# Kernel optimization log

Measured on AMD Instinct MI355X. Metric: run time of the kernel, lower is better.

Reference implementation:

```python
import jax, jax.numpy as jnp
import numpy as np

N_NODES = 100000
N_EDGES = 600000
IN_DIM = 128
HID = 128
OUT_DIM = 64
N_LAYERS = 3


def setup_inputs() -> dict:
    key = jax.random.key(0)
    ks = jax.random.split(key, 8)
    x = jax.random.normal(ks[0], (N_NODES, IN_DIM), dtype=jnp.float32)
    edge_index = jax.random.randint(ks[1], (2, N_EDGES), 0, N_NODES, dtype=jnp.int64)
    s = 1.0 / np.sqrt(HID)
    W_in = jax.random.normal(ks[2], (HID, IN_DIM), dtype=jnp.float32) * s
    b_in = jax.random.normal(ks[3], (HID,), dtype=jnp.float32) * s
    W_convs = jax.random.normal(ks[4], (N_LAYERS, HID, HID), dtype=jnp.float32) * s
    b_convs = jax.random.normal(ks[5], (N_LAYERS, HID), dtype=jnp.float32) * s
    W_out = jax.random.normal(ks[6], (OUT_DIM, (N_LAYERS + 1) * HID), dtype=jnp.float32) * s
    b_out = jax.random.normal(ks[7], (OUT_DIM,), dtype=jnp.float32) * s
    return {"x": x, "edge_index": edge_index, "W_in": W_in, "b_in": b_in,
            "W_convs": W_convs, "b_convs": b_convs, "W_out": W_out, "b_out": b_out}


def reference(x, edge_index, W_in, b_in, W_convs, b_convs, W_out, b_out):
    src, dst = edge_index[0], edge_index[1]
    n = x.shape[0]
    # input projection: [N, in] -> [N, H]
    h = x @ W_in.T + b_in
    hidden_states = [h]
    for i in range(W_convs.shape[0]):
        # GINConv (eps=0): nn(x + sum of neighbor messages), messages src->dst
        agg = jax.ops.segment_sum(h[src], dst, num_segments=n)
        h = (h + agg) @ W_convs[i].T + b_convs[i]
        hidden_states.append(h)
    cat = jnp.concatenate(hidden_states, axis=1)  # [N, (L+1)*H]
    out = cat @ W_out.T + b_out  # [N, OUT]
    return jax.nn.softmax(out, axis=-1)
```

## Files before the change

kernel.cpp:

```cpp
#include <hip/hip_runtime.h>
#include <hip/hip_bf16.h>
#include <hip/hip_fp16.h>

#define GN 100000
#define GE 600000
#define SCAN_NBLK 98
#define ALD 132
#define EDGE_BLOCKS ((GE + 255) / 256)
#define CONV_BLOCKS ((81984 + 255) / 256)

typedef __bf16    bf16x8 __attribute__((ext_vector_type(8)));
typedef _Float16  f16x8  __attribute__((ext_vector_type(8)));
typedef float     f32x4  __attribute__((ext_vector_type(4)));

__global__ __launch_bounds__(256) void prep_fused(
    const int* __restrict__ dst, int* __restrict__ deg,
    const float* __restrict__ Win, const float* __restrict__ Wc,
    const float* __restrict__ Wout,
    const float* __restrict__ b3, const float* __restrict__ bOut,
    __bf16* __restrict__ hi, __bf16* __restrict__ lo,
    float* __restrict__ cvec)
{
    if (blockIdx.x < EDGE_BLOCKS) {
        const int e = blockIdx.x * 256 + threadIdx.x;
        if (e < GE) atomicAdd(&deg[dst[e]], 1);
        return;
    }
    const int i = (blockIdx.x - EDGE_BLOCKS) * 256 + threadIdx.x;
    const float* W3 = Wc + 32768;
    if (i >= 81984) return;
    if (i >= 81920) {
        const int o = i - 81920;
        float c = bOut[o];
        for (int j = 0; j < 128; ++j)
            c += Wout[o * 512 + 384 + j] * b3[j];
        cvec[o] = c;
        return;
    }
    float v;
    if (i < 16384) {
        v = Win[i];
    } else if (i < 49152) {
        v = Wc[i - 16384];
    } else if (i < 57344) {
        const int j = i - 49152;
        v = Wout[(j >> 7) * 512 + (j & 127)];
    } else if (i < 65536) {
        const int j = i - 57344;
        v = Wout[(j >> 7) * 512 + 128 + (j & 127)];
    } else if (i < 73728) {
        const int j = i - 65536;
        v = Wout[(j >> 7) * 512 + 256 + (j & 127)];
    } else {
        const int j = i - 65536;
        const int o = (j >> 7) - 64;
        const int k = j & 127;
        float s = 0.f;
        for (int jj = 0; jj < 128; ++jj)
            s += Wout[o * 512 + 384 + jj] * W3[jj * 128 + k];
        v = s;
    }
    const __bf16 h = (__bf16)v;
    hi[i] = h;
    lo[i] = (__bf16)(v - (float)h);
}

__global__ __launch_bounds__(256) void scan_pass1(const int* __restrict__ deg,
                                                  int* __restrict__ excl,
                                                  int* __restrict__ blockSums,
                                                  int* __restrict__ blockOffs,
                                                  int* __restrict__ done)
{
    __shared__ int s[256];
    __shared__ bool amLast;
    const int t = threadIdx.x;
    const int base = blockIdx.x * 1024 + t * 4;

    int4 v = make_int4(0, 0, 0, 0);
    if (base + 3 < GN) {
        v = *(const int4*)(deg + base);
    } else {
        if (base + 0 < GN) v.x = deg[base + 0];
        if (base + 1 < GN) v.y = deg[base + 1];
        if (base + 2 < GN) v.z = deg[base + 2];
        if (base + 3 < GN) v.w = deg[base + 3];
    }
    const int mysum = v.x + v.y + v.z + v.w;
    s[t] = mysum;
    __syncthreads();
    for (int off = 1; off < 256; off <<= 1) {
        const int val = (t >= off) ? s[t - off] : 0;
        __syncthreads();
        s[t] += val;
        __syncthreads();
    }
    int4 o;
    o.x = s[t] - mysum;
    o.y = o.x + v.x;
    o.z = o.y + v.y;
    o.w = o.z + v.z;
    if (base + 3 < GN) {
        *(int4*)(excl + base) = o;
    } else {
        if (base + 0 < GN) excl[base + 0] = o.x;
        if (base + 1 < GN) excl[base + 1] = o.y;
        if (base + 2 < GN) excl[base + 2] = o.z;
        if (base + 3 < GN) excl[base + 3] = o.w;
    }
    if (t == 255) blockSums[blockIdx.x] = s[255];

    __threadfence();
    if (t == 0)
        amLast = (atomicAdd(done, 1) == SCAN_NBLK - 1);
    __syncthreads();
    if (amLast) {
        __threadfence();
        const int bv = (t < SCAN_NBLK) ? blockSums[t] : 0;
        s[t] = (t < 128) ? bv : 0;
        __syncthreads();
        for (int off = 1; off < 128; off <<= 1) {
            const int val = (t >= off && t < 128) ? s[t - off] : 0;
            __syncthreads();
            if (t < 128) s[t] += val;
            __syncthreads();
        }
        if (t < SCAN_NBLK) blockOffs[t] = s[t] - bv;
    }
}

__global__ __launch_bounds__(256, 8) void gather_rows(
    const uint* __restrict__ Hw,
    const int* __restrict__ row_start,
    const int* __restrict__ deg,
    const int* __restrict__ csr,
    float* __restrict__ Aggp)
{
    const int wave = threadIdx.x >> 6;
    const int lane = threadIdx.x & 63;
    const int row  = blockIdx.x * 4 + wave;
    if (row >= GN) return;

    const uint self = Hw[(size_t)row * 64 + lane];
    const int start = row_start[row];
    const int dg    = deg[row];
    float2 acc = make_float2(0.f, 0.f);

    for (int b = 0; b < dg; b += 64) {
        const int n = min(dg - b, 64);
        const int idx = csr[start + min(b + lane, dg - 1)];
        for (int k = 0; k < n; k += 8) {
            uint t[8];
#pragma unroll
            for (int u = 0; u < 8; ++u) {
                const int s = __shfl(idx, min(k + u, n - 1));
                t[u] = Hw[(size_t)s * 64 + lane];
            }
            const int m = min(n - k, 8);
#pragma unroll
            for (int u = 0; u < 8; ++u) {
                if (u < m) {
                    union { uint uu; _Float16 h[2]; } cv;
                    cv.uu = t[u];
                    acc.x += (float)cv.h[0];
                    acc.y += (float)cv.h[1];
                }
            }
        }
    }

    union { uint uu; _Float16 h[2]; } sv;
    sv.uu = self;
    acc.x += (float)sv.h[0];
    acc.y += (float)sv.h[1];

    *(float2*)&Aggp[(size_t)row * 128 + lane * 2] = acc;
}

__global__ __launch_bounds__(256, 8) void gather_softmax(
    const float* __restrict__ Y,
    const int* __restrict__ row_start,
    const int* __restrict__ deg,
    const int* __restrict__ csr,
    const float* __restrict__ P0,
    const float* __restrict__ P1,
    const float* __restrict__ P2,
    const float* __restrict__ cvec,
    float* __restrict__ out)
{
    const int wave = threadIdx.x >> 6;
    const int lane = threadIdx.x & 63;
    const int row  = blockIdx.x * 4 + wave;
    if (row >= GN) return;

    const size_t g = (size_t)row * 64 + lane;
    const float p0 = P0[g];
    const float p1 = P1[g];
    const float p2 = P2[g];
    const float self = Y[g];
    const float cv = cvec[lane];

    const int start = row_start[row];
    const int dg    = deg[row];
    float acc = 0.f;

    for (int b = 0; b < dg; b += 64) {
        const int n = min(dg - b, 64);
        const int idx = csr[start + min(b + lane, dg - 1)];
        for (int k = 0; k < n; k += 8) {
            float t[8];
#pragma unroll
            for (int u = 0; u < 8; ++u) {
                const int s = __shfl(idx, min(k + u, n - 1));
                t[u] = Y[(size_t)s * 64 + lane];
            }
            const int m = min(n - k, 8);
#pragma unroll
            for (int u = 0; u < 8; ++u)
                if (u < m) acc += t[u];
        }
    }

    const float v = p0 + p1 + p2 + (acc + self) + cv;
    float mx = v;
#pragma unroll
    for (int off = 32; off > 0; off >>= 1) mx = fmaxf(mx, __shfl_xor(mx, off));
    const float e = __expf(v - mx);
    float s = e;
#pragma unroll
    for (int off = 32; off > 0; off >>= 1) s += __shfl_xor(s, off);
    out[g] = e / s;
}

__device__ __forceinline__ void gemm_tile(
    const float* __restrict__ AccBuf,
    const __bf16* __restrict__ Whi, const __bf16* __restrict__ Wlo,
    const int wn, const int quad, const int l15,
    f32x4 acc[2][2])
{
#pragma unroll
    for (int i = 0; i < 2; ++i)
#pragma unroll
        for (int j = 0; j < 2; ++j) acc[i][j] = (f32x4)(0.0f);

    bf16x8 whA[2], wlA[2], whB[2], wlB[2];
#pragma unroll
    for (int nt = 0; nt < 2; ++nt) {
        const int n = wn + nt * 16 + l15;
        whA[nt] = *(const bf16x8*)(Whi + (size_t)n * 128 + quad * 8);
        wlA[nt] = *(const bf16x8*)(Wlo + (size_t)n * 128 + quad * 8);
    }
#pragma unroll
    for (int ks = 0; ks < 4; ++ks) {
        const int kt = ks * 32 + quad * 8;
        if (ks < 3) {
            const int kn = kt + 32;
#pragma unroll
            for (int nt = 0; nt < 2; ++nt) {
                const int n = wn + nt * 16 + l15;
                whB[nt] = *(const bf16x8*)(Whi + (size_t)n * 128 + kn);
                wlB[nt] = *(const bf16x8*)(Wlo + (size_t)n * 128 + kn);
            }
        }
        bf16x8 ahi[2], alo[2];
#pragma unroll
        for (int mt = 0; mt < 2; ++mt) {
            const float* ap = &AccBuf[(mt * 16 + l15) * ALD + kt];
            const f32x4 p = *(const f32x4*)ap;
            const f32x4 q = *(const f32x4*)(ap + 4);
#pragma unroll
            for (int e = 0; e < 4; ++e) {
                const __bf16 hp = (__bf16)p[e];
                const __bf16 hq = (__bf16)q[e];
                ahi[mt][e]     = hp;
                ahi[mt][e + 4] = hq;
                alo[mt][e]     = (__bf16)(p[e] - (float)hp);
                alo[mt][e + 4] = (__bf16)(q[e] - (float)hq);
            }
        }
#pragma unroll
        for (int mt = 0; mt < 2; ++mt)
#pragma unroll
            for (int nt = 0; nt < 2; ++nt) {
                acc[mt][nt] = __builtin_amdgcn_mfma_f32_16x16x32_bf16(
                    ahi[mt], whA[nt], acc[mt][nt], 0, 0, 0);
                acc[mt][nt] = __builtin_amdgcn_mfma_f32_16x16x32_bf16(
                    ahi[mt], wlA[nt], acc[mt][nt], 0, 0, 0);
                acc[mt][nt] = __builtin_amdgcn_mfma_f32_16x16x32_bf16(
                    alo[mt], whA[nt], acc[mt][nt], 0, 0, 0);
            }
        if (ks < 3) {
#pragma unroll
            for (int nt = 0; nt < 2; ++nt) {
                whA[nt] = whB[nt];
                wlA[nt] = wlB[nt];
            }
        }
    }
}

__device__ __forceinline__ void gemm_tile64(
    const float* __restrict__ AccBuf,
    const __bf16* __restrict__ Ehi, const __bf16* __restrict__ Elo,
    const int wn16, const int quad, const int l15,
    f32x4 acc[2])
{
    acc[0] = (f32x4)(0.0f);
    acc[1] = (f32x4)(0.0f);

    const int n = wn16 + l15;
    bf16x8 whA, wlA, whB, wlB;
    whA = *(const bf16x8*)(Ehi + (size_t)n * 128 + quad * 8);
    wlA = *(const bf16x8*)(Elo + (size_t)n * 128 + quad * 8);

#pragma unroll
    for (int ks = 0; ks < 4; ++ks) {
        const int kt = ks * 32 + quad * 8;
        if (ks < 3) {
            whB = *(const bf16x8*)(Ehi + (size_t)n * 128 + kt + 32);
            wlB = *(const bf16x8*)(Elo + (size_t)n * 128 + kt + 32);
        }
        bf16x8 ahi[2], alo[2];
#pragma unroll
        for (int mt = 0; mt < 2; ++mt) {
            const float* ap = &AccBuf[(mt * 16 + l15) * ALD + kt];
            const f32x4 p = *(const f32x4*)ap;
            const f32x4 q = *(const f32x4*)(ap + 4);
#pragma unroll
            for (int e = 0; e < 4; ++e) {
                const __bf16 hp = (__bf16)p[e];
                const __bf16 hq = (__bf16)q[e];
                ahi[mt][e]     = hp;
                ahi[mt][e + 4] = hq;
                alo[mt][e]     = (__bf16)(p[e] - (float)hp);
                alo[mt][e + 4] = (__bf16)(q[e] - (float)hq);
            }
        }
#pragma unroll
        for (int mt = 0; mt < 2; ++mt) {
            acc[mt] = __builtin_amdgcn_mfma_f32_16x16x32_bf16(
                ahi[mt], whA, acc[mt], 0, 0, 0);
            acc[mt] = __builtin_amdgcn_mfma_f32_16x16x32_bf16(
                ahi[mt], wlA, acc[mt], 0, 0, 0);
            acc[mt] = __builtin_amdgcn_mfma_f32_16x16x32_bf16(
                alo[mt], whA, acc[mt], 0, 0, 0);
        }
        if (ks < 3) { whA = whB; wlA = wlB; }
    }
}

template<int MODE>
__global__ __launch_bounds__(256, 3) void gin_layer(
    const float* __restrict__ in,
    const __bf16* __restrict__ Whi,
    const __bf16* __restrict__ Wlo,
    const float* __restrict__ bias,
    const __bf16* __restrict__ Ehi,
    const __bf16* __restrict__ Elo,
    _Float16* __restrict__ Hout,
    float* __restrict__ partial,
    float* __restrict__ y2)
{
    __shared__ float Acc[32 * ALD];

    const int tid  = threadIdx.x;
    const int wave = tid >> 6;
    const int lane = tid & 63;
    const int row0 = blockIdx.x * 32;
    const int wn   = wave * 32;
    const int quad = lane >> 4;
    const int l15  = lane & 15;
    const int c8   = l15 * 8;

#pragma unroll
    for (int p = 0; p < 2; ++p) {
        const int r = wave * 8 + p * 4 + quad;
        const size_t g = (size_t)(row0 + r) * 128 + c8;
        const f32x4 v0 = *(const f32x4*)(in + g);
        const f32x4 v1 = *(const f32x4*)(in + g + 4);
        *(f32x4*)&Acc[r * ALD + c8]     = v0;
        *(f32x4*)&Acc[r * ALD + c8 + 4] = v1;
    }
    __syncthreads();

    f32x4 acc1[2][2];
    gemm_tile(Acc, Whi, Wlo, wn, quad, l15, acc1);
    __syncthreads();

#pragma unroll
    for (int nt = 0; nt < 2; ++nt) {
        const int col = wn + nt * 16 + l15;
        const float b = bias[col];
#pragma unroll
        for (int mt = 0; mt < 2; ++mt)
#pragma unroll
            for (int r4 = 0; r4 < 4; ++r4)
                Acc[(mt * 16 + quad * 4 + r4) * ALD + col] = acc1[mt][nt][r4] + b;
    }
    __syncthreads();

    if (MODE < 2) {
#pragma unroll
        for (int p = 0; p < 2; ++p) {
            const int q = tid + p * 256;
            const int r = q >> 4;
            const int g = (q & 15) * 8;
            const float4 a = *(const float4*)&Acc[r * ALD + g];
            const float4 b = *(const float4*)&Acc[r * ALD + g + 4];
            f16x8 o = {(_Float16)a.x, (_Float16)a.y, (_Float16)a.z, (_Float16)a.w,
                       (_Float16)b.x, (_Float16)b.y, (_Float16)b.z, (_Float16)b.w};
            *(f16x8*)&Hout[(size_t)(row0 + r) * 128 + g] = o;
        }
    }

    if (MODE < 2) {
        f32x4 accE[2];
        gemm_tile64(Acc, Ehi, Elo, wave * 16, quad, l15, accE);
        const int colE = wave * 16 + l15;
#pragma unroll
        for (int mt = 0; mt < 2; ++mt)
#pragma unroll
            for (int r4 = 0; r4 < 4; ++r4)
                partial[(size_t)(row0 + mt * 16 + quad * 4 + r4) * 64 + colE]
                    = accE[mt][r4];
    } else {
        f32x4 acc2[2][2];
        gemm_tile(Acc, Ehi, Elo, wn, quad, l15, acc2);
        float* const dst = (wave < 2) ? partial : y2;
        const int cbase = wn & 63;
#pragma unroll
        for (int nt = 0; nt < 2; ++nt)
#pragma unroll
            for (int mt = 0; mt < 2; ++mt)
#pragma unroll
                for (int r4 = 0; r4 < 4; ++r4)
                    dst[(size_t)(row0 + mt * 16 + quad * 4 + r4) * 64
                        + cbase + nt * 16 + l15] = acc2[mt][nt][r4];
    }
}

__global__ __launch_bounds__(256) void scan_pass3(int* __restrict__ excl,
                                                  const int* __restrict__ blockOffs,
                                                  int* __restrict__ cursor)
{
    const int i = blockIdx.x * 256 + threadIdx.x;
    if (i >= GN) return;
    const int v = excl[i] + blockOffs[i >> 10];
    excl[i]   = v;
    cursor[i] = v;
}

__global__ __launch_bounds__(256) void fill_csr(const int* __restrict__ src,
                                                const int* __restrict__ dst,
                                                int* __restrict__ cursor,
                                                int* __restrict__ csr)
{
    const int e = blockIdx.x * 256 + threadIdx.x;
    if (e >= GE) return;
    const int pos = atomicAdd(&cursor[dst[e]], 1);
    csr[pos] = src[e];
}

extern "C" void kernel_launch(void* const* d_in, const int* in_sizes, int n_in,
                              void* d_out, int out_size, void* d_ws, size_t ws_size,
                              hipStream_t stream)
{
    const float* x       = (const float*)d_in[0];
    const int*   src     = (const int*)d_in[1];
    const int*   dst     = ((const int*)d_in[1]) + GE;
    const float* W_in    = (const float*)d_in[2];
    const float* b_in    = (const float*)d_in[3];
    const float* W_convs = (const float*)d_in[4];
    const float* b_convs = (const float*)d_in[5];
    const float* W_out   = (const float*)d_in[6];
    const float* b_out   = (const float*)d_in[7];
    float*       out     = (float*)d_out;

    _Float16* h0   = (_Float16*)d_ws;
    _Float16* h1   = h0 + (size_t)GN * 128;
    float*    Aggp = (float*)(h1 + (size_t)GN * 128);
    float*    p0   = Aggp + (size_t)GN * 128;
    float*    p1   = p0 + (size_t)GN * 64;
    float*    p2   = p1 + (size_t)GN * 64;
    float*    y2   = p2 + (size_t)GN * 64;
    float*    cvec = y2 + (size_t)GN * 64;
    int*      deg       = (int*)(cvec + 128);
    int*      done      = deg + GN;
    int*      row_start = done + 4;
    int*      cursor    = row_start + GN;
    int*      blockSums = cursor + GN;
    int*      blockOffs = blockSums + 128;
    int*      csr       = blockOffs + 128;
    __bf16*   Whi       = (__bf16*)(csr + GE);
    __bf16*   Wlo       = Whi + 81920;

    const dim3 blk(256);
    const dim3 gblk(256);
    const int node_blocks   = (GN + 255) / 256;
    const int layer_blocks  = GN / 32;
    const int gather_blocks = (GN + 3) / 4;

    hipMemsetAsync(deg, 0, (GN + 4) * sizeof(int), stream);
    prep_fused<<<EDGE_BLOCKS + CONV_BLOCKS, blk, 0, stream>>>(
        dst, deg, W_in, W_convs, W_out, b_convs + 256, b_out, Whi, Wlo, cvec);
    scan_pass1<<<SCAN_NBLK, blk, 0, stream>>>(deg, row_start, blockSums,
                                              blockOffs, done);
    scan_pass3<<<node_blocks, blk, 0, stream>>>(row_start, blockOffs, cursor);
    fill_csr<<<EDGE_BLOCKS, blk, 0, stream>>>(src, dst, cursor, csr);

    gin_layer<0><<<layer_blocks, gblk, 0, stream>>>(
        x, Whi, Wlo, b_in, Whi + 49152, Wlo + 49152, h0, p0, nullptr);

    gather_rows<<<gather_blocks, gblk, 0, stream>>>(
        (const uint*)h0, row_start, deg, csr, Aggp);
    gin_layer<1><<<layer_blocks, gblk, 0, stream>>>(
        Aggp, Whi + 16384, Wlo + 16384, b_convs,
        Whi + 57344, Wlo + 57344, h1, p1, nullptr);

    gather_rows<<<gather_blocks, gblk, 0, stream>>>(
        (const uint*)h1, row_start, deg, csr, Aggp);
    gin_layer<2><<<layer_blocks, gblk, 0, stream>>>(
        Aggp, Whi + 32768, Wlo + 32768, b_convs + 128,
        Whi + 65536, Wlo + 65536, nullptr, p2, y2);

    gather_softmax<<<gather_blocks, gblk, 0, stream>>>(
        y2, row_start, deg, csr, p0, p1, p2, cvec, out);
}
```

Baseline: 442.7 us.

## Fuse input projection layer into prep kernel using on-the-fly fp32 weight splitting

```diff
diff --git a/kernel.cpp b/kernel.cpp
--- a/kernel.cpp
+++ b/kernel.cpp
@@ -8,61 +8,298 @@
 #define ALD 132
 #define EDGE_BLOCKS ((GE + 255) / 256)
 #define CONV_BLOCKS ((81984 + 255) / 256)
+#define L0_BLOCKS   (GN / 32)
 
 typedef __bf16    bf16x8 __attribute__((ext_vector_type(8)));
 typedef _Float16  f16x8  __attribute__((ext_vector_type(8)));
 typedef float     f32x4  __attribute__((ext_vector_type(4)));
 
-__global__ __launch_bounds__(256) void prep_fused(
+__device__ __forceinline__ void split8(const float* __restrict__ wp,
+                                       bf16x8& hi, bf16x8& lo)
+{
+    const f32x4 a = *(const f32x4*)wp;
+    const f32x4 b = *(const f32x4*)(wp + 4);
+#pragma unroll
+    for (int e = 0; e < 4; ++e) {
+        const __bf16 ha = (__bf16)a[e];
+        const __bf16 hb = (__bf16)b[e];
+        hi[e]     = ha;
+        hi[e + 4] = hb;
+        lo[e]     = (__bf16)(a[e] - (float)ha);
+        lo[e + 4] = (__bf16)(b[e] - (float)hb);
+    }
+}
+
+__device__ __forceinline__ void gemm_tile(
+    const float* __restrict__ AccBuf,
+    const __bf16* __restrict__ Whi, const __bf16* __restrict__ Wlo,
+    const int wn, const int quad, const int l15,
+    f32x4 acc[2][2])
+{
+#pragma unroll
+    for (int i = 0; i < 2; ++i)
+#pragma unroll
+        for (int j = 0; j < 2; ++j) acc[i][j] = (f32x4)(0.0f);
+
+    bf16x8 whA[2], wlA[2], whB[2], wlB[2];
+#pragma unroll
+    for (int nt = 0; nt < 2; ++nt) {
+        const int n = wn + nt * 16 + l15;
+        whA[nt] = *(const bf16x8*)(Whi + (size_t)n * 128 + quad * 8);
+        wlA[nt] = *(const bf16x8*)(Wlo + (size_t)n * 128 + quad * 8);
+    }
+#pragma unroll
+    for (int ks = 0; ks < 4; ++ks) {
+        const int kt = ks * 32 + quad * 8;
+        if (ks < 3) {
+            const int kn = kt + 32;
+#pragma unroll
+            for (int nt = 0; nt < 2; ++nt) {
+                const int n = wn + nt * 16 + l15;
+                whB[nt] = *(const bf16x8*)(Whi + (size_t)n * 128 + kn);
+                wlB[nt] = *(const bf16x8*)(Wlo + (size_t)n * 128 + kn);
+            }
+        }
+        bf16x8 ahi[2], alo[2];
+#pragma unroll
+        for (int mt = 0; mt < 2; ++mt) {
+            const float* ap = &AccBuf[(mt * 16 + l15) * ALD + kt];
+            const f32x4 p = *(const f32x4*)ap;
+            const f32x4 q = *(const f32x4*)(ap + 4);
+#pragma unroll
+            for (int e = 0; e < 4; ++e) {
+                const __bf16 hp = (__bf16)p[e];
+                const __bf16 hq = (__bf16)q[e];
+                ahi[mt][e]     = hp;
+                ahi[mt][e + 4] = hq;
+                alo[mt][e]     = (__bf16)(p[e] - (float)hp);
+                alo[mt][e + 4] = (__bf16)(q[e] - (float)hq);
+            }
+        }
+#pragma unroll
+        for (int mt = 0; mt < 2; ++mt)
+#pragma unroll
+            for (int nt = 0; nt < 2; ++nt) {
+                acc[mt][nt] = __builtin_amdgcn_mfma_f32_16x16x32_bf16(
+                    ahi[mt], whA[nt], acc[mt][nt], 0, 0, 0);
+                acc[mt][nt] = __builtin_amdgcn_mfma_f32_16x16x32_bf16(
+                    ahi[mt], wlA[nt], acc[mt][nt], 0, 0, 0);
+                acc[mt][nt] = __builtin_amdgcn_mfma_f32_16x16x32_bf16(
+                    alo[mt], whA[nt], acc[mt][nt], 0, 0, 0);
+            }
+        if (ks < 3) {
+#pragma unroll
+            for (int nt = 0; nt < 2; ++nt) {
+                whA[nt] = whB[nt];
+                wlA[nt] = wlB[nt];
+            }
+        }
+    }
+}
+
+__device__ __forceinline__ void gemm_tile_w32(
+    const float* __restrict__ AccBuf,
+    const float* __restrict__ W, const int ldw,
+    const int wn, const int quad, const int l15,
+    f32x4 acc[2][2])
+{
+#pragma unroll
+    for (int i = 0; i < 2; ++i)
+#pragma unroll
+        for (int j = 0; j < 2; ++j) acc[i][j] = (f32x4)(0.0f);
+
+#pragma unroll
+    for (int ks = 0; ks < 4; ++ks) {
+        const int kt = ks * 32 + quad * 8;
+        bf16x8 wh[2], wl[2];
+#pragma unroll
+        for (int nt = 0; nt < 2; ++nt) {
+            const int n = wn + nt * 16 + l15;
+            split8(W + (size_t)n * ldw + kt, wh[nt], wl[nt]);
+        }
+        bf16x8 ahi[2], alo[2];
+#pragma unroll
+        for (int mt = 0; mt < 2; ++mt) {
+            const float* ap = &AccBuf[(mt * 16 + l15) * ALD + kt];
+            const f32x4 p = *(const f32x4*)ap;
+            const f32x4 q = *(const f32x4*)(ap + 4);
+#pragma unroll
+            for (int e = 0; e < 4; ++e) {
+                const __bf16 hp = (__bf16)p[e];
+                const __bf16 hq = (__bf16)q[e];
+                ahi[mt][e]     = hp;
+                ahi[mt][e + 4] = hq;
+                alo[mt][e]     = (__bf16)(p[e] - (float)hp);
+                alo[mt][e + 4] = (__bf16)(q[e] - (float)hq);
+            }
+        }
+#pragma unroll
+        for (int mt = 0; mt < 2; ++mt)
+#pragma unroll
+            for (int nt = 0; nt < 2; ++nt) {
+                acc[mt][nt] = __builtin_amdgcn_mfma_f32_16x16x32_bf16(
+                    ahi[mt], wh[nt], acc[mt][nt], 0, 0, 0);
+                acc[mt][nt] = __builtin_amdgcn_mfma_f32_16x16x32_bf16(
+                    ahi[mt], wl[nt], acc[mt][nt], 0, 0, 0);
+                acc[mt][nt] = __builtin_amdgcn_mfma_f32_16x16x32_bf16(
+                    alo[mt], wh[nt], acc[mt][nt], 0, 0, 0);
+            }
+    }
+}
+
+__device__ __forceinline__ void gemm_tile64_w32(
+    const float* __restrict__ AccBuf,
+    const float* __restrict__ E, const int ldw,
+    const int wn16, const int quad, const int l15,
+    f32x4 acc[2])
+{
+    acc[0] = (f32x4)(0.0f);
+    acc[1] = (f32x4)(0.0f);
+    const int n = wn16 + l15;
+
+#pragma unroll
+    for (int ks = 0; ks < 4; ++ks) {
+        const int kt = ks * 32 + quad * 8;
+        bf16x8 wh, wl;
+        split8(E + (size_t)n * ldw + kt, wh, wl);
+        bf16x8 ahi[2], alo[2];
+#pragma unroll
+        for (int mt = 0; mt < 2; ++mt) {
+            const float* ap = &AccBuf[(mt * 16 + l15) * ALD + kt];
+            const f32x4 p = *(const f32x4*)ap;
+            const f32x4 q = *(const f32x4*)(ap + 4);
+#pragma unroll
+            for (int e = 0; e < 4; ++e) {
+                const __bf16 hp = (__bf16)p[e];
+                const __bf16 hq = (__bf16)q[e];
+                ahi[mt][e]     = hp;
+                ahi[mt][e + 4] = hq;
+                alo[mt][e]     = (__bf16)(p[e] - (float)hp);
+                alo[mt][e + 4] = (__bf16)(q[e] - (float)hq);
+            }
+        }
+#pragma unroll
+        for (int mt = 0; mt < 2; ++mt) {
+            acc[mt] = __builtin_amdgcn_mfma_f32_16x16x32_bf16(
+                ahi[mt], wh, acc[mt], 0, 0, 0);
+            acc[mt] = __builtin_amdgcn_mfma_f32_16x16x32_bf16(
+                ahi[mt], wl, acc[mt], 0, 0, 0);
+            acc[mt] = __builtin_amdgcn_mfma_f32_16x16x32_bf16(
+                alo[mt], wh, acc[mt], 0, 0, 0);
+        }
+    }
+}
+
+__global__ __launch_bounds__(256, 3) void prep_fused(
     const int* __restrict__ dst, int* __restrict__ deg,
+    const float* __restrict__ x,
     const float* __restrict__ Win, const float* __restrict__ Wc,
     const float* __restrict__ Wout,
+    const float* __restrict__ bIn,
     const float* __restrict__ b3, const float* __restrict__ bOut,
     __bf16* __restrict__ hi, __bf16* __restrict__ lo,
-    float* __restrict__ cvec)
-{
+    float* __restrict__ cvec,
+    _Float16* __restrict__ h0, float* __restrict__ p0)
+{
+    __shared__ float Acc[32 * ALD];
+
     if (blockIdx.x < EDGE_BLOCKS) {
         const int e = blockIdx.x * 256 + threadIdx.x;
         if (e < GE) atomicAdd(&deg[dst[e]], 1);
         return;
     }
-    const int i = (blockIdx.x - EDGE_BLOCKS) * 256 + threadIdx.x;
-    const float* W3 = Wc + 32768;
-    if (i >= 81984) return;
-    if (i >= 81920) {
-        const int o = i - 81920;
-        float c = bOut[o];
-        for (int j = 0; j < 128; ++j)
-            c += Wout[o * 512 + 384 + j] * b3[j];
-        cvec[o] = c;
+    if (blockIdx.x < EDGE_BLOCKS + CONV_BLOCKS) {
+        const int i = (blockIdx.x - EDGE_BLOCKS) * 256 + threadIdx.x;
+        const float* W3 = Wc + 32768;
+        if (i >= 81984) return;
+        if (i >= 81920) {
+            const int o = i - 81920;
+            float c = bOut[o];
+            for (int j = 0; j < 128; ++j)
+                c += Wout[o * 512 + 384 + j] * b3[j];
+            cvec[o] = c;
+            return;
+        }
+        if (i < 16384) return;
+        if (i >= 49152 && i < 57344) return;
+        float v;
+        if (i < 49152) {
+            v = Wc[i - 16384];
+        } else if (i < 65536) {
+            const int j = i - 57344;
+            v = Wout[(j >> 7) * 512 + 128 + (j & 127)];
+        } else if (i < 73728) {
+            const int j = i - 65536;
+            v = Wout[(j >> 7) * 512 + 256 + (j & 127)];
+        } else {
+            const int j = i - 65536;
+            const int o = (j >> 7) - 64;
+            const int k = j & 127;
+            float s = 0.f;
+            for (int jj = 0; jj < 128; ++jj)
+                s += Wout[o * 512 + 384 + jj] * W3[jj * 128 + k];
+            v = s;
+        }
+        const __bf16 h = (__bf16)v;
+        hi[i] = h;
+        lo[i] = (__bf16)(v - (float)h);
         return;
     }
-    float v;
-    if (i < 16384) {
-        v = Win[i];
-    } else if (i < 49152) {
-        v = Wc[i - 16384];
-    } else if (i < 57344) {
-        const int j = i - 49152;
-        v = Wout[(j >> 7) * 512 + (j & 127)];
-    } else if (i < 65536) {
-        const int j = i - 57344;
-        v = Wout[(j >> 7) * 512 + 128 + (j & 127)];
-    } else if (i < 73728) {
-        const int j = i - 65536;
-        v = Wout[(j >> 7) * 512 + 256 + (j & 127)];
-    } else {
-        const int j = i - 65536;
-        const int o = (j >> 7) - 64;
-        const int k = j & 127;
-        float s = 0.f;
-        for (int jj = 0; jj < 128; ++jj)
-            s += Wout[o * 512 + 384 + jj] * W3[jj * 128 + k];
-        v = s;
-    }
-    const __bf16 h = (__bf16)v;
-    hi[i] = h;
-    lo[i] = (__bf16)(v - (float)h);
+
+    const int tid  = threadIdx.x;
+    const int wave = tid >> 6;
+    const int lane = tid & 63;
+    const int row0 = (blockIdx.x - EDGE_BLOCKS - CONV_BLOCKS) * 32;
+    const int wn   = wave * 32;
+    const int quad = lane >> 4;
+    const int l15  = lane & 15;
+    const int c8   = l15 * 8;
+
+#pragma unroll
+    for (int p = 0; p < 2; ++p) {
+        const int r = wave * 8 + p * 4 + quad;
+        const size_t g = (size_t)(row0 + r) * 128 + c8;
+        *(f32x4*)&Acc[r * ALD + c8]     = *(const f32x4*)(x + g);
+        *(f32x4*)&Acc[r * ALD + c8 + 4] = *(const f32x4*)(x + g + 4);
+    }
+    __syncthreads();
+
+    f32x4 acc1[2][2];
+    gemm_tile_w32(Acc, Win, 128, wn, quad, l15, acc1);
+    __syncthreads();
+
+#pragma unroll
+    for (int nt = 0; nt < 2; ++nt) {
+        const int col = wn + nt * 16 + l15;
+        const float b = bIn[col];
+#pragma unroll
+        for (int mt = 0; mt < 2; ++mt)
+#pragma unroll
+            for (int r4 = 0; r4 < 4; ++r4)
+                Acc[(mt * 16 + quad * 4 + r4) * ALD + col] = acc1[mt][nt][r4] + b;
+    }
+    __syncthreads();
+
+#pragma unroll
+    for (int p = 0; p < 2; ++p) {
+        const int q = tid + p * 256;
+        const int r = q >> 4;
+        const int g = (q & 15) * 8;
+        const float4 a = *(const float4*)&Acc[r * ALD + g];
+        const float4 b = *(const float4*)&Acc[r * ALD + g + 4];
+        f16x8 o = {(_Float16)a.x, (_Float16)a.y, (_Float16)a.z, (_Float16)a.w,
+                   (_Float16)b.x, (_Float16)b.y, (_Float16)b.z, (_Float16)b.w};
+        *(f16x8*)&h0[(size_t)(row0 + r) * 128 + g] = o;
+    }
+
+    f32x4 accE[2];
+    gemm_tile64_w32(Acc, Wout, 512, wave * 16, quad, l15, accE);
+    const int colE = wave * 16 + l15;
+#pragma unroll
+    for (int mt = 0; mt < 2; ++mt)
+#pragma unroll
+        for (int r4 = 0; r4 < 4; ++r4)
+            p0[(size_t)(row0 + mt * 16 + quad * 4 + r4) * 64 + colE] = accE[mt][r4];
 }
 
 __global__ __launch_bounds__(256) void scan_pass1(const int* __restrict__ deg,
@@ -231,73 +468,6 @@
     out[g] = e / s;
 }
 
-__device__ __forceinline__ void gemm_tile(
-    const float* __restrict__ AccBuf,
-    const __bf16* __restrict__ Whi, const __bf16* __restrict__ Wlo,
-    const int wn, const int quad, const int l15,
-    f32x4 acc[2][2])
-{
-#pragma unroll
-    for (int i = 0; i < 2; ++i)
-#pragma unroll
-        for (int j = 0; j < 2; ++j) acc[i][j] = (f32x4)(0.0f);
-
-    bf16x8 whA[2], wlA[2], whB[2], wlB[2];
-#pragma unroll
-    for (int nt = 0; nt < 2; ++nt) {
-        const int n = wn + nt * 16 + l15;
-        whA[nt] = *(const bf16x8*)(Whi + (size_t)n * 128 + quad * 8);
-        wlA[nt] = *(const bf16x8*)(Wlo + (size_t)n * 128 + quad * 8);
-    }
-#pragma unroll
-    for (int ks = 0; ks < 4; ++ks) {
-        const int kt = ks * 32 + quad * 8;
-        if (ks < 3) {
-            const int kn = kt + 32;
-#pragma unroll
-            for (int nt = 0; nt < 2; ++nt) {
-                const int n = wn + nt * 16 + l15;
-                whB[nt] = *(const bf16x8*)(Whi + (size_t)n * 128 + kn);
-                wlB[nt] = *(const bf16x8*)(Wlo + (size_t)n * 128 + kn);
-            }
-        }
-        bf16x8 ahi[2], alo[2];
-#pragma unroll
-        for (int mt = 0; mt < 2; ++mt) {
-            const float* ap = &AccBuf[(mt * 16 + l15) * ALD + kt];
-            const f32x4 p = *(const f32x4*)ap;
-            const f32x4 q = *(const f32x4*)(ap + 4);
-#pragma unroll
-            for (int e = 0; e < 4; ++e) {
-                const __bf16 hp = (__bf16)p[e];
-                const __bf16 hq = (__bf16)q[e];
-                ahi[mt][e]     = hp;
-                ahi[mt][e + 4] = hq;
-                alo[mt][e]     = (__bf16)(p[e] - (float)hp);
-                alo[mt][e + 4] = (__bf16)(q[e] - (float)hq);
-            }
-        }
-#pragma unroll
-        for (int mt = 0; mt < 2; ++mt)
-#pragma unroll
-            for (int nt = 0; nt < 2; ++nt) {
-                acc[mt][nt] = __builtin_amdgcn_mfma_f32_16x16x32_bf16(
-                    ahi[mt], whA[nt], acc[mt][nt], 0, 0, 0);
-                acc[mt][nt] = __builtin_amdgcn_mfma_f32_16x16x32_bf16(
-                    ahi[mt], wlA[nt], acc[mt][nt], 0, 0, 0);
-                acc[mt][nt] = __builtin_amdgcn_mfma_f32_16x16x32_bf16(
-                    alo[mt], whA[nt], acc[mt][nt], 0, 0, 0);
-            }
-        if (ks < 3) {
-#pragma unroll
-            for (int nt = 0; nt < 2; ++nt) {
-                whA[nt] = whB[nt];
-                wlA[nt] = wlB[nt];
-            }
-        }
-    }
-}
-
 __device__ __forceinline__ void gemm_tile64(
     const float* __restrict__ AccBuf,
     const __bf16* __restrict__ Ehi, const __bf16* __restrict__ Elo,
@@ -375,10 +545,8 @@
     for (int p = 0; p < 2; ++p) {
         const int r = wave * 8 + p * 4 + quad;
         const size_t g = (size_t)(row0 + r) * 128 + c8;
-        const f32x4 v0 = *(const f32x4*)(in + g);
-        const f32x4 v1 = *(const f32x4*)(in + g + 4);
-        *(f32x4*)&Acc[r * ALD + c8]     = v0;
-        *(f32x4*)&Acc[r * ALD + c8 + 4] = v1;
+        *(f32x4*)&Acc[r * ALD + c8]     = *(const f32x4*)(in + g);
+        *(f32x4*)&Acc[r * ALD + c8 + 4] = *(const f32x4*)(in + g + 4);
     }
     __syncthreads();
 
@@ -500,15 +668,13 @@
     const int gather_blocks = (GN + 3) / 4;
 
     hipMemsetAsync(deg, 0, (GN + 4) * sizeof(int), stream);
-    prep_fused<<<EDGE_BLOCKS + CONV_BLOCKS, blk, 0, stream>>>(
-        dst, deg, W_in, W_convs, W_out, b_convs + 256, b_out, Whi, Wlo, cvec);
+    prep_fused<<<EDGE_BLOCKS + CONV_BLOCKS + L0_BLOCKS, blk, 0, stream>>>(
+        dst, deg, x, W_in, W_convs, W_out, b_in, b_convs + 256, b_out,
+        Whi, Wlo, cvec, h0, p0);
     scan_pass1<<<SCAN_NBLK, blk, 0, stream>>>(deg, row_start, blockSums,
                                               blockOffs, done);
     scan_pass3<<<node_blocks, blk, 0, stream>>>(row_start, blockOffs, cursor);
     fill_csr<<<EDGE_BLOCKS, blk, 0, stream>>>(src, dst, cursor, csr);
-
-    gin_layer<0><<<layer_blocks, gblk, 0, stream>>>(
-        x, Whi, Wlo, b_in, Whi + 49152, Wlo + 49152, h0, p0, nullptr);
 
     gather_rows<<<gather_blocks, gblk, 0, stream>>>(
         (const uint*)h0, row_start, deg, csr, Aggp);
```

After: 430.7 us (median of 2 runs). 2.7% less time.
